# Kernel tuning notes

Measured on AMD Instinct MI355X. Metric: run time of the kernel, lower is better.

The kernel has to match this reference:

```python
import jax, jax.numpy as jnp
import numpy as np

B, S, H, D = 2, 256, 8, 32
TOTAL = H * D          # Config.total = 256
FF = 4 * TOTAL         # Config.ff = 1024
MAXSEP = 256           # Config.max_sep_len
L = 2                  # num_layers
EPS = 1e-5

def sinusoidal_table(max_sep_len, dim):
    # matches get_embedding(rel_pos_init=0)
    num = 2 * max_sep_len + 1
    half = dim // 2
    freq = np.exp(np.arange(half, dtype=np.float32) * (-(np.log(10000.0) / (half - 1))))
    ang = np.arange(num, dtype=np.float32)[:, None] * freq[None, :]
    emb = np.concatenate([np.sin(ang), np.cos(ang)], axis=1).reshape(num, -1)
    return jnp.asarray(emb, dtype=jnp.float32)

def ln(x):
    # fresh nn.LayerNorm each call in the source => default gamma=1, beta=0
    m = jnp.mean(x, axis=-1, keepdims=True)
    v = jnp.mean(jnp.square(x - m), axis=-1, keepdims=True)
    return (x - m) / jnp.sqrt(v + EPS)

def setup_inputs() -> dict:
    key = jax.random.key(0)
    ks = jax.random.split(key, 16)
    p = lambda k, shp: (jax.random.normal(k, shp, jnp.float32) * 0.02)
    return {
        "x": jax.random.normal(ks[0], (B, S, TOTAL), jnp.float32),
        "pos_s": jax.random.randint(ks[1], (B, S), 0, MAXSEP, dtype=jnp.int32),
        "pos_e": jax.random.randint(ks[2], (B, S), 0, MAXSEP, dtype=jnp.int32),
        "real_lengths": jax.random.randint(ks[3], (B,), 1, S + 1, dtype=jnp.int32),
        "lex_num": 0,
        # learned rel-pos table (sinusoidal init); four_pos_shared => one table for ss/se/es/ee
        "pe": sinusoidal_table(MAXSEP, TOTAL),
        "W_fus": p(ks[4], (4 * TOTAL, TOTAL)),
        "b_fus": jnp.zeros((TOTAL,), jnp.float32),
        "Wq": p(ks[5], (L, TOTAL, TOTAL)), "bq": jnp.zeros((L, TOTAL), jnp.float32),
        "Wk": p(ks[6], (L, TOTAL, TOTAL)), "bk": jnp.zeros((L, TOTAL), jnp.float32),
        "Wv": p(ks[7], (L, TOTAL, TOTAL)), "bv": jnp.zeros((L, TOTAL), jnp.float32),
        "Wr": p(ks[8], (L, TOTAL, TOTAL)), "br": jnp.zeros((L, TOTAL), jnp.float32),
        "u": p(ks[9], (L, H, D)), "v": p(ks[10], (L, H, D)),
        "W1": p(ks[11], (L, TOTAL, FF)), "b1": jnp.zeros((L, FF), jnp.float32),
        "W2": p(ks[12], (L, FF, TOTAL)), "b2": jnp.zeros((L, TOTAL), jnp.float32),
    }

def reference(x, pos_s, pos_e, real_lengths, lex_num, pe, W_fus, b_fus,
              Wq, bq, Wk, bk, Wv, bv, Wr, br, u, v, W1, b1, W2, b2):
    # key mask: seq_len_to_mask(real_lengths + lex_num)
    mask = jnp.arange(S)[None, :] < (real_lengths + lex_num)[:, None]  # [B,S]
    # ---- Get_four_embedding (mode != 'ff_two'): 4-way lattice fusion ----
    dss = pos_s[:, :, None] - pos_s[:, None, :] + MAXSEP
    dse = pos_s[:, :, None] - pos_e[:, None, :] + MAXSEP
    des = pos_e[:, :, None] - pos_s[:, None, :] + MAXSEP
    dee = pos_e[:, :, None] - pos_e[:, None, :] + MAXSEP
    four = jnp.concatenate([pe[dss], pe[dse], pe[des], pe[dee]], axis=-1)  # [B,S,S,4T]
    rel = jax.nn.relu(four @ W_fus + b_fus)                                # [B,S,S,T]
    out = x
    for l in range(L):
        q = (out @ Wq[l] + bq[l]).reshape(B, S, H, D)
        k = (out @ Wk[l] + bk[l]).reshape(B, S, H, D)
        val = (out @ Wv[l] + bv[l]).reshape(B, S, H, D)
        r = (rel @ Wr[l] + br[l]).reshape(B, S, S, H, D)
        # A_C = (q + u) k^T ; B_D = (q + v) . rel[i,j]   (no 1/sqrt(d) scaling in source)
        AC = jnp.einsum('bihd,bjhd->bhij', q + u[l], k)
        BD = jnp.einsum('bihd,bijhd->bhij', q + v[l], r)
        score = jnp.where(mask[:, None, None, :], AC + BD, -1e15)
        prob = jax.nn.softmax(score, axis=-1)
        attn = jnp.einsum('bhij,bjhd->bihd', prob, val).reshape(B, S, TOTAL)
        y = ln(out + attn)                      # post-attn residual + LayerNorm
        # Positionwise_Feedforward: Linear-ReLU-Linear-ReLU (ReLU after 2nd linear too), residual, LN
        h = jax.nn.relu(y @ W1[l] + b1[l])
        z = jax.nn.relu(h @ W2[l] + b2[l])
        out = ln(z + y)
    return out
```

## Files before the change

### kernel.cpp

```cpp
#include <hip/hip_runtime.h>
#include <hip/hip_fp16.h>
#include <math.h>

#define NH 8
#define NDIST 513

union H8 { uint4 u4; __half2 h2[4]; };

__device__ __forceinline__ void gemm4(const float4* __restrict__ w0, int ld4,
                                      const float* ldsA, float* red, int tid) {
  int cg = tid & 63, ks = tid >> 6;
  const float4* w = w0 + (ks * 64) * ld4 + cg;
  float a00=0,a01=0,a02=0,a03=0, a10=0,a11=0,a12=0,a13=0,
        a20=0,a21=0,a22=0,a23=0, a30=0,a31=0,a32=0,a33=0;
  const float* A = ldsA + ks * 64;
  #pragma unroll 4
  for (int kk = 0; kk < 64; ++kk) {
    float4 b4 = w[kk * ld4];
    float x0 = A[kk], x1 = A[256 + kk], x2 = A[512 + kk], x3 = A[768 + kk];
    a00=fmaf(x0,b4.x,a00); a01=fmaf(x0,b4.y,a01); a02=fmaf(x0,b4.z,a02); a03=fmaf(x0,b4.w,a03);
    a10=fmaf(x1,b4.x,a10); a11=fmaf(x1,b4.y,a11); a12=fmaf(x1,b4.z,a12); a13=fmaf(x1,b4.w,a13);
    a20=fmaf(x2,b4.x,a20); a21=fmaf(x2,b4.y,a21); a22=fmaf(x2,b4.z,a22); a23=fmaf(x2,b4.w,a23);
    a30=fmaf(x3,b4.x,a30); a31=fmaf(x3,b4.y,a31); a32=fmaf(x3,b4.z,a32); a33=fmaf(x3,b4.w,a33);
  }
  float* rp = red + ks * 1024 + cg * 4;
  *(float4*)(rp)       = make_float4(a00,a01,a02,a03);
  *(float4*)(rp + 256) = make_float4(a10,a11,a12,a13);
  *(float4*)(rp + 512) = make_float4(a20,a21,a22,a23);
  *(float4*)(rp + 768) = make_float4(a30,a31,a32,a33);
}

__device__ __forceinline__ float redsum(const float* red, int r, int c) {
  return red[r*256+c] + red[1024 + r*256+c] + red[2048 + r*256+c] + red[3072 + r*256+c];
}

__device__ __forceinline__ void ln_write(float val, float* red2, float* dst, int tid) {
  float ss = val;
  #pragma unroll
  for (int sh = 32; sh >= 1; sh >>= 1) ss += __shfl_xor(ss, sh);
  if ((tid & 63) == 0) red2[tid >> 6] = ss;
  __syncthreads();
  float mean = (red2[0] + red2[1] + red2[2] + red2[3]) * (1.f / 256.f);
  float d = val - mean;
  float s2 = d * d;
  __syncthreads();
  #pragma unroll
  for (int sh = 32; sh >= 1; sh >>= 1) s2 += __shfl_xor(s2, sh);
  if ((tid & 63) == 0) red2[tid >> 6] = s2;
  __syncthreads();
  float var = (red2[0] + red2[1] + red2[2] + red2[3]) * (1.f / 256.f);
  dst[tid] = d * rsqrtf(var + 1e-5f);
}

__global__ void k_setup(const float* __restrict__ pe, const float* __restrict__ W_fus,
                        const float* __restrict__ b_fus, const float* __restrict__ x,
                        const float* __restrict__ Wq, const float* __restrict__ Wk,
                        const float* __restrict__ Wv, const float* __restrict__ bq,
                        const float* __restrict__ bk, const float* __restrict__ bv,
                        const float* __restrict__ uu, __half* __restrict__ Tt,
                        float* __restrict__ QU, float* __restrict__ Kb,
                        float* __restrict__ Vb) {
  __shared__ float smem[5120];
  float* ldsA = smem; float* red = smem + 1024;
  int tid = threadIdx.x, bx = blockIdx.x;
  if (bx < 516) {
    int g = bx & 3, r0 = (bx >> 2) * 4;
    #pragma unroll
    for (int t = 0; t < 4; ++t) {
      int idx = t * 256 + tid, r = idx >> 8, c = idx & 255;
      int row = r0 + r;
      ldsA[idx] = (row < NDIST) ? pe[row * 256 + c] : 0.f;
    }
    __syncthreads();
    gemm4((const float4*)(W_fus + g * 65536), 64, ldsA, red, tid);
    __syncthreads();
    float bb = (g == 0) ? b_fus[tid] : 0.f;
    #pragma unroll
    for (int r = 0; r < 4; ++r) {
      int row = r0 + r;
      if (row < NDIST)
        Tt[(g * NDIST + row) * 256 + tid] = __float2half(bb + redsum(red, r, tid));
    }
  } else {
    int pb = bx - 516;
    int by = pb / 128, r0 = (pb % 128) * 4;
    const float* W = (by == 0) ? Wq : (by == 1) ? Wk : Wv;
    #pragma unroll
    for (int t = 0; t < 4; ++t) {
      int idx = t * 256 + tid, r = idx >> 8, c = idx & 255;
      ldsA[idx] = x[(r0 + r) * 256 + c];
    }
    __syncthreads();
    gemm4((const float4*)W, 64, ldsA, red, tid);
    __syncthreads();
    #pragma unroll
    for (int r = 0; r < 4; ++r) {
      int row = r0 + r;
      float s = redsum(red, r, tid);
      if (by == 0)      QU[row * 256 + tid] = s + bq[tid] + uu[tid];
      else if (by == 1) Kb[row * 256 + tid] = s + bk[tid];
      else              Vb[row * 256 + tid] = s + bv[tid];
    }
  }
}

__global__ void k_proj(const float* __restrict__ cur, const float* __restrict__ Wq,
                       const float* __restrict__ Wk, const float* __restrict__ Wv,
                       const float* __restrict__ bq, const float* __restrict__ bk,
                       const float* __restrict__ bv, const float* __restrict__ uu,
                       float* __restrict__ QU, float* __restrict__ Kb,
                       float* __restrict__ Vb) {
  __shared__ float smem[5120];
  float* ldsA = smem; float* red = smem + 1024;
  int tid = threadIdx.x;
  int r0 = blockIdx.x * 4;
  int by = blockIdx.y;
  const float* W = (by == 0) ? Wq : (by == 1) ? Wk : Wv;
  #pragma unroll
  for (int t = 0; t < 4; ++t) {
    int idx = t * 256 + tid, r = idx >> 8, c = idx & 255;
    ldsA[idx] = cur[(r0 + r) * 256 + c];
  }
  __syncthreads();
  gemm4((const float4*)W, 64, ldsA, red, tid);
  __syncthreads();
  #pragma unroll
  for (int r = 0; r < 4; ++r) {
    int row = r0 + r;
    float s = redsum(red, r, tid);
    if (by == 0)      QU[row * 256 + tid] = s + bq[tid] + uu[tid];
    else if (by == 1) Kb[row * 256 + tid] = s + bk[tid];
    else              Vb[row * 256 + tid] = s + bv[tid];
  }
}

__global__ void k_attn(const float* __restrict__ QU, const float* __restrict__ Kb,
                       const float* __restrict__ Vb, const float* __restrict__ Wr,
                       const float* __restrict__ uvec, const float* __restrict__ vvec,
                       const __half* __restrict__ Tt, const float* __restrict__ cur,
                       const int* __restrict__ pos_s, const int* __restrict__ pos_e,
                       const int* __restrict__ real_lengths, const int* __restrict__ lex_num,
                       float* __restrict__ Y) {
  __shared__ __align__(16) float smem[4896];
  int tid = threadIdx.x;
  int bi = blockIdx.x, b = bi >> 8, i = bi & 255;
  int rl = real_lengths[b] + lex_num[0];
  float* sc    = smem;
  __half* plh  = (__half*)(smem + 2048);
  float* qu    = smem + 3072;
  float* part  = smem + 3328;
  float* inv8  = smem + 4352;
  float* red2  = smem + 4360;
  float* scl   = smem + 4368;
  float* qv    = smem + 4624;
  #pragma unroll
  for (int t = 0; t < 8; ++t) sc[t * 256 + tid] = -1e15f;
  {
    float q = QU[bi * 256 + tid];
    qu[tid] = q;
    qv[tid] = q - uvec[tid] + vvec[tid];
  }
  __syncthreads();
  {
    const float4* wrp = (const float4*)(Wr + tid * 256);
    #pragma unroll
    for (int h = 0; h < NH; ++h) {
      float acc = 0.f;
      #pragma unroll
      for (int q8 = 0; q8 < 8; ++q8) {
        float4 w = wrp[h * 8 + q8];
        const float* qq = qv + h * 32 + q8 * 4;
        acc += w.x * qq[0] + w.y * qq[1] + w.z * qq[2] + w.w * qq[3];
      }
      plh[h * 256 + tid] = __float2half(acc);
    }
  }
  __syncthreads();
  int psi = pos_s[b*256 + i], pei = pos_e[b*256 + i];
  int jl = tid >> 3, cl = tid & 7;
  int nchunk = (rl + 31) >> 5;
  for (int jc = 0; jc < nchunk; ++jc) {
    int j = jc * 32 + jl;
    int psj = pos_s[b*256 + j], pej = pos_e[b*256 + j];
    const __half* t0 = Tt + (psi - psj + 256) * 256;
    const __half* t1 = Tt + (NDIST   + (psi - pej + 256)) * 256;
    const __half* t2 = Tt + (2*NDIST + (pei - psj + 256)) * 256;
    const __half* t3 = Tt + (3*NDIST + (pei - pej + 256)) * 256;
    __half2 z2 = __float2half2_rn(0.f);
    __half2 acc2[NH];
    #pragma unroll
    for (int h = 0; h < NH; ++h) acc2[h] = z2;
    #pragma unroll
    for (int ci = 0; ci < 4; ++ci) {
      int c0 = (ci * 8 + cl) * 8;
      H8 A0, A1, A2, A3;
      A0.u4 = *(const uint4*)(t0 + c0);
      A1.u4 = *(const uint4*)(t1 + c0);
      A2.u4 = *(const uint4*)(t2 + c0);
      A3.u4 = *(const uint4*)(t3 + c0);
      __half2 r2[4];
      #pragma unroll
      for (int p = 0; p < 4; ++p) {
        __half2 s = __hadd2(__hadd2(A0.h2[p], A1.h2[p]), __hadd2(A2.h2[p], A3.h2[p]));
        r2[p] = __hmul2(s, __hgt2(s, z2));
      }
      #pragma unroll
      for (int h = 0; h < NH; ++h) {
        H8 Ph;
        Ph.u4 = *(const uint4*)(plh + h*256 + c0);
        #pragma unroll
        for (int p = 0; p < 4; ++p) acc2[h] = __hfma2(r2[p], Ph.h2[p], acc2[h]);
      }
    }
    const float4* kp = (const float4*)(Kb + (b*256 + j) * 256);
    float bd[NH];
    #pragma unroll
    for (int h = 0; h < NH; ++h) {
      bd[h] = __low2float(acc2[h]) + __high2float(acc2[h]);
      float4 k4 = kp[h*8 + cl];
      float4 q4 = *(const float4*)(qu + h*32 + cl*4);
      bd[h] += k4.x*q4.x + k4.y*q4.y + k4.z*q4.z + k4.w*q4.w;
    }
    #pragma unroll
    for (int h = 0; h < NH; ++h) {
      bd[h] += __shfl_xor(bd[h], 1);
      bd[h] += __shfl_xor(bd[h], 2);
      bd[h] += __shfl_xor(bd[h], 4);
    }
    if (cl == 0) {
      #pragma unroll
      for (int h = 0; h < NH; ++h) scl[h*32 + jl] = bd[h];
    }
    __syncthreads();
    { int h = tid >> 5, jj = tid & 31, j2 = jc * 32 + jj;
      if (j2 < rl) sc[h*256 + j2] = scl[h*32 + jj]; }
    __syncthreads();
  }
  {
    int h = tid >> 5, t = tid & 31;
    float mx = -INFINITY;
    #pragma unroll
    for (int m = 0; m < 8; ++m) mx = fmaxf(mx, sc[h*256 + t + 32*m]);
    #pragma unroll
    for (int sh = 16; sh >= 1; sh >>= 1) mx = fmaxf(mx, __shfl_xor(mx, sh));
    float sum = 0.f;
    #pragma unroll
    for (int m = 0; m < 8; ++m) {
      float e = __expf(sc[h*256 + t + 32*m] - mx);
      sc[h*256 + t + 32*m] = e;
      sum += e;
    }
    #pragma unroll
    for (int sh = 16; sh >= 1; sh >>= 1) sum += __shfl_xor(sum, sh);
    if (t == 0) inv8[h] = 1.f / sum;
  }
  __syncthreads();
  {
    int n4 = tid & 63, jg = tid >> 6, h = n4 >> 3;
    float4 acc = make_float4(0.f, 0.f, 0.f, 0.f);
    if (jg * 64 < rl) {
      const float4* vp = (const float4*)(Vb + b * 65536) + n4;
      #pragma unroll 4
      for (int jj0 = 0; jj0 < 64; ++jj0) {
        int jj = jg * 64 + jj0;
        float s = sc[h*256 + jj];
        float4 v4 = vp[jj * 64];
        acc.x = fmaf(s, v4.x, acc.x); acc.y = fmaf(s, v4.y, acc.y);
        acc.z = fmaf(s, v4.z, acc.z); acc.w = fmaf(s, v4.w, acc.w);
      }
    }
    *(float4*)(part + jg*256 + n4*4) = acc;
  }
  __syncthreads();
  int n = tid;
  float o = part[n] + part[256+n] + part[512+n] + part[768+n];
  float val = cur[bi*256 + n] + o * inv8[n >> 5];
  ln_write(val, red2, Y + bi*256, tid);
}

__global__ void k_ffn1(const float* __restrict__ Y, const float* __restrict__ W1,
                       const float* __restrict__ b1, float* __restrict__ H1) {
  __shared__ float smem[5120];
  float* ldsA = smem; float* red = smem + 1024;
  int tid = threadIdx.x;
  int r0 = blockIdx.x * 4, by = blockIdx.y;
  #pragma unroll
  for (int t = 0; t < 4; ++t) {
    int idx = t * 256 + tid, r = idx >> 8, c = idx & 255;
    ldsA[idx] = Y[(r0 + r) * 256 + c];
  }
  __syncthreads();
  gemm4((const float4*)W1 + by * 64, 256, ldsA, red, tid);
  __syncthreads();
  int n = by * 256 + tid;
  float bb = b1[n];
  #pragma unroll
  for (int r = 0; r < 4; ++r)
    H1[(r0 + r) * 1024 + n] = fmaxf(bb + redsum(red, r, tid), 0.f);
}

__global__ void k_ffn2(const float* __restrict__ H1, const float* __restrict__ W2,
                       float* __restrict__ Pbuf) {
  __shared__ float smem[5120];
  float* ldsA = smem; float* red = smem + 1024;
  int tid = threadIdx.x;
  int r0 = blockIdx.x * 4, kc = blockIdx.y, k0 = kc * 256;
  #pragma unroll
  for (int t = 0; t < 4; ++t) {
    int idx = t * 256 + tid, r = idx >> 8, c = idx & 255;
    ldsA[idx] = H1[(r0 + r) * 1024 + k0 + c];
  }
  __syncthreads();
  gemm4((const float4*)(W2 + k0 * 256), 64, ldsA, red, tid);
  __syncthreads();
  #pragma unroll
  for (int r = 0; r < 4; ++r)
    Pbuf[kc * 131072 + (r0 + r) * 256 + tid] = redsum(red, r, tid);
}

__global__ void k_ffn2red_ln(const float* __restrict__ Pbuf, const float* __restrict__ b2,
                             const float* __restrict__ Y, float* __restrict__ O) {
  __shared__ float red2[4];
  int m = blockIdx.x, tid = threadIdx.x;
  float s = Pbuf[m * 256 + tid] + Pbuf[131072 + m * 256 + tid] +
            Pbuf[262144 + m * 256 + tid] + Pbuf[393216 + m * 256 + tid] + b2[tid];
  float val = fmaxf(s, 0.f) + Y[m * 256 + tid];
  ln_write(val, red2, O + m * 256, tid);
}

extern "C" void kernel_launch(void* const* d_in, const int* in_sizes, int n_in,
                              void* d_out, int out_size, void* d_ws, size_t ws_size,
                              hipStream_t stream) {
  const float* x            = (const float*)d_in[0];
  const int*   pos_s        = (const int*)d_in[1];
  const int*   pos_e        = (const int*)d_in[2];
  const int*   real_lengths = (const int*)d_in[3];
  const int*   lex_num      = (const int*)d_in[4];
  const float* pe           = (const float*)d_in[5];
  const float* W_fus        = (const float*)d_in[6];
  const float* b_fus        = (const float*)d_in[7];
  const float* Wq           = (const float*)d_in[8];
  const float* bq           = (const float*)d_in[9];
  const float* Wk           = (const float*)d_in[10];
  const float* bk           = (const float*)d_in[11];
  const float* Wv           = (const float*)d_in[12];
  const float* bv           = (const float*)d_in[13];
  const float* Wr           = (const float*)d_in[14];
  const float* u            = (const float*)d_in[16];
  const float* v            = (const float*)d_in[17];
  const float* W1           = (const float*)d_in[18];
  const float* b1           = (const float*)d_in[19];
  const float* W2           = (const float*)d_in[20];
  const float* b2           = (const float*)d_in[21];
  float* out = (float*)d_out;

  float* ws = (float*)d_ws;
  __half* Tt = (__half*)ws;
  float* QU  = ws + 262656;
  float* Kb  = QU + 131072;
  float* Vb  = Kb + 131072;
  float* Y   = Vb + 131072;
  float* C1  = Y + 131072;
  float* H1  = C1 + 131072;
  float* Pb  = H1 + 524288;

  k_setup<<<900, 256, 0, stream>>>(pe, W_fus, b_fus, x, Wq, Wk, Wv, bq, bk, bv,
                                   u, Tt, QU, Kb, Vb);
  k_attn<<<512, 256, 0, stream>>>(QU, Kb, Vb, Wr, u, v, Tt, x, pos_s, pos_e,
                                  real_lengths, lex_num, Y);
  k_ffn1<<<dim3(128, 4), 256, 0, stream>>>(Y, W1, b1, H1);
  k_ffn2<<<dim3(128, 4), 256, 0, stream>>>(H1, W2, Pb);
  k_ffn2red_ln<<<512, 256, 0, stream>>>(Pb, b2, Y, C1);
  k_proj<<<dim3(128, 3), 256, 0, stream>>>(C1, Wq + 65536, Wk + 65536, Wv + 65536,
                                           bq + 256, bk + 256, bv + 256, u + 256,
                                           QU, Kb, Vb);
  k_attn<<<512, 256, 0, stream>>>(QU, Kb, Vb, Wr + 65536, u + 256, v + 256, Tt, C1,
                                  pos_s, pos_e, real_lengths, lex_num, Y);
  k_ffn1<<<dim3(128, 4), 256, 0, stream>>>(Y, W1 + 262144, b1 + 1024, H1);
  k_ffn2<<<dim3(128, 4), 256, 0, stream>>>(H1, W2 + 262144, Pb);
  k_ffn2red_ln<<<512, 256, 0, stream>>>(Pb, b2 + 256, Y, out);
}
```

Before: 127.8 us.

## Hoist q·Wr projection into separate batched kernel and halve GEMM row tiles

Moves the per-row (q+v)·Wr^T projection out of the attention kernel into a new k_p kernel. k_p stages each Wr head slice in shared memory and reuses it across 4 query rows, then writes fp16 results to a workspace buffer that k_attn loads with one vector copy. Before, every attention block streamed the full 256 KB Wr matrix. All fp32 GEMM kernels also drop from 4 rows to 2 rows per block, doubling grid sizes for more parallelism at the cost of less weight reuse. It adds two kernel launches and an extra global round trip for P.

```diff
diff --git a/kernel.cpp b/kernel.cpp
--- a/kernel.cpp
+++ b/kernel.cpp
@@ -7,31 +7,26 @@
 
 union H8 { uint4 u4; __half2 h2[4]; };
 
-__device__ __forceinline__ void gemm4(const float4* __restrict__ w0, int ld4,
+__device__ __forceinline__ void gemm2(const float4* __restrict__ w0, int ld4,
                                       const float* ldsA, float* red, int tid) {
   int cg = tid & 63, ks = tid >> 6;
   const float4* w = w0 + (ks * 64) * ld4 + cg;
-  float a00=0,a01=0,a02=0,a03=0, a10=0,a11=0,a12=0,a13=0,
-        a20=0,a21=0,a22=0,a23=0, a30=0,a31=0,a32=0,a33=0;
+  float a00=0,a01=0,a02=0,a03=0, a10=0,a11=0,a12=0,a13=0;
   const float* A = ldsA + ks * 64;
   #pragma unroll 4
   for (int kk = 0; kk < 64; ++kk) {
     float4 b4 = w[kk * ld4];
-    float x0 = A[kk], x1 = A[256 + kk], x2 = A[512 + kk], x3 = A[768 + kk];
+    float x0 = A[kk], x1 = A[256 + kk];
     a00=fmaf(x0,b4.x,a00); a01=fmaf(x0,b4.y,a01); a02=fmaf(x0,b4.z,a02); a03=fmaf(x0,b4.w,a03);
     a10=fmaf(x1,b4.x,a10); a11=fmaf(x1,b4.y,a11); a12=fmaf(x1,b4.z,a12); a13=fmaf(x1,b4.w,a13);
-    a20=fmaf(x2,b4.x,a20); a21=fmaf(x2,b4.y,a21); a22=fmaf(x2,b4.z,a22); a23=fmaf(x2,b4.w,a23);
-    a30=fmaf(x3,b4.x,a30); a31=fmaf(x3,b4.y,a31); a32=fmaf(x3,b4.z,a32); a33=fmaf(x3,b4.w,a33);
-  }
-  float* rp = red + ks * 1024 + cg * 4;
+  }
+  float* rp = red + ks * 512 + cg * 4;
   *(float4*)(rp)       = make_float4(a00,a01,a02,a03);
   *(float4*)(rp + 256) = make_float4(a10,a11,a12,a13);
-  *(float4*)(rp + 512) = make_float4(a20,a21,a22,a23);
-  *(float4*)(rp + 768) = make_float4(a30,a31,a32,a33);
-}
-
-__device__ __forceinline__ float redsum(const float* red, int r, int c) {
-  return red[r*256+c] + red[1024 + r*256+c] + red[2048 + r*256+c] + red[3072 + r*256+c];
+}
+
+__device__ __forceinline__ float redsum2(const float* red, int r, int c) {
+  return red[r*256+c] + red[512 + r*256+c] + red[1024 + r*256+c] + red[1536 + r*256+c];
 }
 
 __device__ __forceinline__ void ln_write(float val, float* red2, float* dst, int tid) {
@@ -60,43 +55,43 @@
                         const float* __restrict__ uu, __half* __restrict__ Tt,
                         float* __restrict__ QU, float* __restrict__ Kb,
                         float* __restrict__ Vb) {
-  __shared__ float smem[5120];
-  float* ldsA = smem; float* red = smem + 1024;
+  __shared__ float smem[2560];
+  float* ldsA = smem; float* red = smem + 512;
   int tid = threadIdx.x, bx = blockIdx.x;
-  if (bx < 516) {
-    int g = bx & 3, r0 = (bx >> 2) * 4;
-    #pragma unroll
-    for (int t = 0; t < 4; ++t) {
+  if (bx < 1028) {
+    int g = bx & 3, r0 = (bx >> 2) * 2;
+    #pragma unroll
+    for (int t = 0; t < 2; ++t) {
       int idx = t * 256 + tid, r = idx >> 8, c = idx & 255;
       int row = r0 + r;
       ldsA[idx] = (row < NDIST) ? pe[row * 256 + c] : 0.f;
     }
     __syncthreads();
-    gemm4((const float4*)(W_fus + g * 65536), 64, ldsA, red, tid);
+    gemm2((const float4*)(W_fus + g * 65536), 64, ldsA, red, tid);
     __syncthreads();
     float bb = (g == 0) ? b_fus[tid] : 0.f;
     #pragma unroll
-    for (int r = 0; r < 4; ++r) {
+    for (int r = 0; r < 2; ++r) {
       int row = r0 + r;
       if (row < NDIST)
-        Tt[(g * NDIST + row) * 256 + tid] = __float2half(bb + redsum(red, r, tid));
+        Tt[(g * NDIST + row) * 256 + tid] = __float2half(bb + redsum2(red, r, tid));
     }
   } else {
-    int pb = bx - 516;
-    int by = pb / 128, r0 = (pb % 128) * 4;
+    int pb = bx - 1028;
+    int by = pb >> 8, r0 = (pb & 255) * 2;
     const float* W = (by == 0) ? Wq : (by == 1) ? Wk : Wv;
     #pragma unroll
-    for (int t = 0; t < 4; ++t) {
+    for (int t = 0; t < 2; ++t) {
       int idx = t * 256 + tid, r = idx >> 8, c = idx & 255;
       ldsA[idx] = x[(r0 + r) * 256 + c];
     }
     __syncthreads();
-    gemm4((const float4*)W, 64, ldsA, red, tid);
-    __syncthreads();
-    #pragma unroll
-    for (int r = 0; r < 4; ++r) {
+    gemm2((const float4*)W, 64, ldsA, red, tid);
+    __syncthreads();
+    #pragma unroll
+    for (int r = 0; r < 2; ++r) {
       int row = r0 + r;
-      float s = redsum(red, r, tid);
+      float s = redsum2(red, r, tid);
       if (by == 0)      QU[row * 256 + tid] = s + bq[tid] + uu[tid];
       else if (by == 1) Kb[row * 256 + tid] = s + bk[tid];
       else              Vb[row * 256 + tid] = s + bv[tid];
@@ -110,38 +105,69 @@
                        const float* __restrict__ bv, const float* __restrict__ uu,
                        float* __restrict__ QU, float* __restrict__ Kb,
                        float* __restrict__ Vb) {
-  __shared__ float smem[5120];
-  float* ldsA = smem; float* red = smem + 1024;
+  __shared__ float smem[2560];
+  float* ldsA = smem; float* red = smem + 512;
   int tid = threadIdx.x;
-  int r0 = blockIdx.x * 4;
+  int r0 = blockIdx.x * 2;
   int by = blockIdx.y;
   const float* W = (by == 0) ? Wq : (by == 1) ? Wk : Wv;
   #pragma unroll
-  for (int t = 0; t < 4; ++t) {
+  for (int t = 0; t < 2; ++t) {
     int idx = t * 256 + tid, r = idx >> 8, c = idx & 255;
     ldsA[idx] = cur[(r0 + r) * 256 + c];
   }
   __syncthreads();
-  gemm4((const float4*)W, 64, ldsA, red, tid);
-  __syncthreads();
-  #pragma unroll
-  for (int r = 0; r < 4; ++r) {
+  gemm2((const float4*)W, 64, ldsA, red, tid);
+  __syncthreads();
+  #pragma unroll
+  for (int r = 0; r < 2; ++r) {
     int row = r0 + r;
-    float s = redsum(red, r, tid);
+    float s = redsum2(red, r, tid);
     if (by == 0)      QU[row * 256 + tid] = s + bq[tid] + uu[tid];
     else if (by == 1) Kb[row * 256 + tid] = s + bk[tid];
     else              Vb[row * 256 + tid] = s + bv[tid];
   }
 }
 
+__global__ void k_p(const float* __restrict__ QU, const float* __restrict__ uvec,
+                    const float* __restrict__ vvec, const float* __restrict__ Wr,
+                    __half* __restrict__ P) {
+  __shared__ float ldsB[32 * 257];
+  __shared__ float ldsA[4 * 32];
+  int rt = blockIdx.x, h = blockIdx.y, tid = threadIdx.x;
+  int r0 = rt * 4;
+  #pragma unroll
+  for (int pass = 0; pass < 8; ++pass) {
+    int c = pass * 32 + (tid >> 3), q = tid & 7;
+    float4 w4 = ((const float4*)(Wr + c * 256 + h * 32))[q];
+    ldsB[(q*4+0)*257 + c] = w4.x; ldsB[(q*4+1)*257 + c] = w4.y;
+    ldsB[(q*4+2)*257 + c] = w4.z; ldsB[(q*4+3)*257 + c] = w4.w;
+  }
+  if (tid < 128) {
+    int r = tid >> 5, d = tid & 31;
+    int col = h * 32 + d;
+    ldsA[r * 32 + d] = QU[(r0 + r) * 256 + col] - uvec[col] + vvec[col];
+  }
+  __syncthreads();
+  int c = tid;
+  float acc[4] = {0, 0, 0, 0};
+  #pragma unroll 4
+  for (int d = 0; d < 32; ++d) {
+    float b = ldsB[d * 257 + c];
+    #pragma unroll
+    for (int r = 0; r < 4; ++r) acc[r] = fmaf(ldsA[r * 32 + d], b, acc[r]);
+  }
+  #pragma unroll
+  for (int r = 0; r < 4; ++r) P[(r0 + r) * 2048 + h * 256 + c] = __float2half(acc[r]);
+}
+
 __global__ void k_attn(const float* __restrict__ QU, const float* __restrict__ Kb,
-                       const float* __restrict__ Vb, const float* __restrict__ Wr,
-                       const float* __restrict__ uvec, const float* __restrict__ vvec,
+                       const float* __restrict__ Vb, const __half* __restrict__ P,
                        const __half* __restrict__ Tt, const float* __restrict__ cur,
                        const int* __restrict__ pos_s, const int* __restrict__ pos_e,
                        const int* __restrict__ real_lengths, const int* __restrict__ lex_num,
                        float* __restrict__ Y) {
-  __shared__ __align__(16) float smem[4896];
+  __shared__ __align__(16) float smem[4640];
   int tid = threadIdx.x;
   int bi = blockIdx.x, b = bi >> 8, i = bi & 255;
   int rl = real_lengths[b] + lex_num[0];
@@ -152,29 +178,10 @@
   float* inv8  = smem + 4352;
   float* red2  = smem + 4360;
   float* scl   = smem + 4368;
-  float* qv    = smem + 4624;
   #pragma unroll
   for (int t = 0; t < 8; ++t) sc[t * 256 + tid] = -1e15f;
-  {
-    float q = QU[bi * 256 + tid];
-    qu[tid] = q;
-    qv[tid] = q - uvec[tid] + vvec[tid];
-  }
-  __syncthreads();
-  {
-    const float4* wrp = (const float4*)(Wr + tid * 256);
-    #pragma unroll
-    for (int h = 0; h < NH; ++h) {
-      float acc = 0.f;
-      #pragma unroll
-      for (int q8 = 0; q8 < 8; ++q8) {
-        float4 w = wrp[h * 8 + q8];
-        const float* qq = qv + h * 32 + q8 * 4;
-        acc += w.x * qq[0] + w.y * qq[1] + w.z * qq[2] + w.w * qq[3];
-      }
-      plh[h * 256 + tid] = __float2half(acc);
-    }
-  }
+  ((uint4*)plh)[tid] = ((const uint4*)(P + bi * 2048))[tid];
+  qu[tid] = QU[bi * 256 + tid];
   __syncthreads();
   int psi = pos_s[b*256 + i], pei = pos_e[b*256 + i];
   int jl = tid >> 3, cl = tid & 7;
@@ -280,42 +287,42 @@
 
 __global__ void k_ffn1(const float* __restrict__ Y, const float* __restrict__ W1,
                        const float* __restrict__ b1, float* __restrict__ H1) {
-  __shared__ float smem[5120];
-  float* ldsA = smem; float* red = smem + 1024;
+  __shared__ float smem[2560];
+  float* ldsA = smem; float* red = smem + 512;
   int tid = threadIdx.x;
-  int r0 = blockIdx.x * 4, by = blockIdx.y;
-  #pragma unroll
-  for (int t = 0; t < 4; ++t) {
+  int r0 = blockIdx.x * 2, by = blockIdx.y;
+  #pragma unroll
+  for (int t = 0; t < 2; ++t) {
     int idx = t * 256 + tid, r = idx >> 8, c = idx & 255;
     ldsA[idx] = Y[(r0 + r) * 256 + c];
   }
   __syncthreads();
-  gemm4((const float4*)W1 + by * 64, 256, ldsA, red, tid);
+  gemm2((const float4*)W1 + by * 64, 256, ldsA, red, tid);
   __syncthreads();
   int n = by * 256 + tid;
   float bb = b1[n];
   #pragma unroll
-  for (int r = 0; r < 4; ++r)
-    H1[(r0 + r) * 1024 + n] = fmaxf(bb + redsum(red, r, tid), 0.f);
+  for (int r = 0; r < 2; ++r)
+    H1[(r0 + r) * 1024 + n] = fmaxf(bb + redsum2(red, r, tid), 0.f);
 }
 
 __global__ void k_ffn2(const float* __restrict__ H1, const float* __restrict__ W2,
                        float* __restrict__ Pbuf) {
-  __shared__ float smem[5120];
-  float* ldsA = smem; float* red = smem + 1024;
+  __shared__ float smem[2560];
+  float* ldsA = smem; float* red = smem + 512;
   int tid = threadIdx.x;
-  int r0 = blockIdx.x * 4, kc = blockIdx.y, k0 = kc * 256;
-  #pragma unroll
-  for (int t = 0; t < 4; ++t) {
+  int r0 = blockIdx.x * 2, kc = blockIdx.y, k0 = kc * 256;
+  #pragma unroll
+  for (int t = 0; t < 2; ++t) {
     int idx = t * 256 + tid, r = idx >> 8, c = idx & 255;
     ldsA[idx] = H1[(r0 + r) * 1024 + k0 + c];
   }
   __syncthreads();
-  gemm4((const float4*)(W2 + k0 * 256), 64, ldsA, red, tid);
-  __syncthreads();
-  #pragma unroll
-  for (int r = 0; r < 4; ++r)
-    Pbuf[kc * 131072 + (r0 + r) * 256 + tid] = redsum(red, r, tid);
+  gemm2((const float4*)(W2 + k0 * 256), 64, ldsA, red, tid);
+  __syncthreads();
+  #pragma unroll
+  for (int r = 0; r < 2; ++r)
+    Pbuf[kc * 131072 + (r0 + r) * 256 + tid] = redsum2(red, r, tid);
 }
 
 __global__ void k_ffn2red_ln(const float* __restrict__ Pbuf, const float* __restrict__ b2,
@@ -359,24 +366,27 @@
   float* QU  = ws + 262656;
   float* Kb  = QU + 131072;
   float* Vb  = Kb + 131072;
-  float* Y   = Vb + 131072;
+  __half* P  = (__half*)(Vb + 131072);
+  float* Y   = Vb + 131072 + 524288;
   float* C1  = Y + 131072;
   float* H1  = C1 + 131072;
   float* Pb  = H1 + 524288;
 
-  k_setup<<<900, 256, 0, stream>>>(pe, W_fus, b_fus, x, Wq, Wk, Wv, bq, bk, bv,
-                                   u, Tt, QU, Kb, Vb);
-  k_attn<<<512, 256, 0, stream>>>(QU, Kb, Vb, Wr, u, v, Tt, x, pos_s, pos_e,
+  k_setup<<<1796, 256, 0, stream>>>(pe, W_fus, b_fus, x, Wq, Wk, Wv, bq, bk, bv,
+                                    u, Tt, QU, Kb, Vb);
+  k_p<<<dim3(128, 8), 256, 0, stream>>>(QU, u, v, Wr, P);
+  k_attn<<<512, 256, 0, stream>>>(QU, Kb, Vb, P, Tt, x, pos_s, pos_e,
                                   real_lengths, lex_num, Y);
-  k_ffn1<<<dim3(128, 4), 256, 0, stream>>>(Y, W1, b1, H1);
-  k_ffn2<<<dim3(128, 4), 256, 0, stream>>>(H1, W2, Pb);
+  k_ffn1<<<dim3(256, 4), 256, 0, stream>>>(Y, W1, b1, H1);
+  k_ffn2<<<dim3(256, 4), 256, 0, stream>>>(H1, W2, Pb);
   k_ffn2red_ln<<<512, 256, 0, stream>>>(Pb, b2, Y, C1);
-  k_proj<<<dim3(128, 3), 256, 0, stream>>>(C1, Wq + 65536, Wk + 65536, Wv + 65536,
+  k_proj<<<dim3(256, 3), 256, 0, stream>>>(C1, Wq + 65536, Wk + 65536, Wv + 65536,
                                            bq + 256, bk + 256, bv + 256, u + 256,
                                            QU, Kb, Vb);
-  k_attn<<<512, 256, 0, stream>>>(QU, Kb, Vb, Wr + 65536, u + 256, v + 256, Tt, C1,
-                                  pos_s, pos_e, real_lengths, lex_num, Y);
-  k_ffn1<<<dim3(128, 4), 256, 0, stream>>>(Y, W1 + 262144, b1 + 1024, H1);
-  k_ffn2<<<dim3(128, 4), 256, 0, stream>>>(H1, W2 + 262144, Pb);
+  k_p<<<dim3(128, 8), 256, 0, stream>>>(QU, u + 256, v + 256, Wr + 65536, P);
+  k_attn<<<512, 256, 0, stream>>>(QU, Kb, Vb, P, Tt, C1, pos_s, pos_e,
+                                  real_lengths, lex_num, Y);
+  k_ffn1<<<dim3(256, 4), 256, 0, stream>>>(Y, W1 + 262144, b1 + 1024, H1);
+  k_ffn2<<<dim3(256, 4), 256, 0, stream>>>(H1, W2 + 262144, Pb);
   k_ffn2red_ln<<<512, 256, 0, stream>>>(Pb, b2 + 256, Y, out);
 }
```

New measurement: 126.4 us. About the same (-1.1%).
